# Optimization experiments

Hardware: AMD Instinct MI355X
Metric: run time of the kernel (lower is better)

## Reference

```python
import jax, jax.numpy as jnp
import numpy as np

B, NPG, DEG = 32, 1024, 16          # graphs, nodes/graph, avg degree
N, E = B * NPG, B * NPG * DEG        # 32768 nodes, 524288 edges
IN_C, HID, H, EDGE_D = 128, 64, 4, 8
RATIO = 0.5
K = int(np.ceil(RATIO * NPG))        # 512 nodes kept per graph (static)
SLOPE = 0.2                          # PyG GATConv LeakyReLU default


def setup_inputs() -> dict:
    key = jax.random.key(0)
    ks = jax.random.split(key, 10)
    x = jax.random.normal(ks[0], (N, IN_C), jnp.float32)
    # edges confined within each graph (block structure like PyG Batch)
    src_l = jax.random.randint(ks[1], (B, NPG * DEG), 0, NPG)
    dst_l = jax.random.randint(ks[2], (B, NPG * DEG), 0, NPG)
    off = (jnp.arange(B) * NPG)[:, None]
    edge_index = jnp.stack([(src_l + off).reshape(-1), (dst_l + off).reshape(-1)]).astype(jnp.int64)
    edge = jax.random.normal(ks[3], (E, EDGE_D), jnp.float32)
    batch_index = jnp.repeat(jnp.arange(B), NPG).astype(jnp.int64)
    s_in = 1.0 / np.sqrt(IN_C)
    W = jax.random.normal(ks[4], (IN_C, H, HID), jnp.float32) * s_in
    a_src = jax.random.normal(ks[5], (H, HID), jnp.float32) * s_in
    a_dst = jax.random.normal(ks[6], (H, HID), jnp.float32) * s_in
    b_gat = jnp.zeros((H * HID,), jnp.float32)
    W_lin = jax.random.normal(ks[7], (H * HID, HID), jnp.float32) * (1.0 / np.sqrt(H * HID))
    b_lin = jnp.zeros((HID,), jnp.float32)
    p_pool = jax.random.normal(ks[8], (HID,), jnp.float32)
    return dict(x=x, edge_index=edge_index, edge=edge, batch_index=batch_index,
                W=W, a_src=a_src, a_dst=a_dst, b_gat=b_gat,
                W_lin=W_lin, b_lin=b_lin, p_pool=p_pool)


def reference(x, edge_index, edge, batch_index, W, a_src, a_dst, b_gat, W_lin, b_lin, p_pool):
    n = x.shape[0]
    # --- GATConv (heads concat, self-loops added, softmax over incoming edges) ---
    loops = jnp.arange(n)
    src = jnp.concatenate([edge_index[0], loops])
    dst = jnp.concatenate([edge_index[1], loops])
    h = jnp.einsum('ni,ihc->nhc', x, W)                  # [N,H,C]
    al_src = (h * a_src).sum(-1)                          # [N,H]
    al_dst = (h * a_dst).sum(-1)                          # [N,H]
    e = jax.nn.leaky_relu(al_src[src] + al_dst[dst], SLOPE)  # [Etot,H]
    m = jax.ops.segment_max(e, dst, num_segments=n)
    ex = jnp.exp(e - m[dst])
    denom = jax.ops.segment_sum(ex, dst, num_segments=n)
    alpha = ex / denom[dst]                               # segment softmax per target
    out = jax.ops.segment_sum(h[src] * alpha[:, :, None], dst, num_segments=n)
    xg = out.reshape(n, H * HID) + b_gat
    # --- Linear ---
    xl = xg @ W_lin + b_lin                               # [N,HID]
    # --- TopKPooling (tanh(x.p/||p||) score, top ceil(ratio*n) per graph) ---
    score = jnp.tanh(xl @ p_pool / jnp.linalg.norm(p_pool))   # [N]
    topv, topi = jax.lax.top_k(score.reshape(B, NPG), K)      # [B,K]
    perm = (topi + (jnp.arange(B) * NPG)[:, None]).reshape(-1)  # global kept node ids
    xp = xl[perm] * topv.reshape(-1)[:, None]             # [B*K,HID], gated by score
    batch_out = jnp.repeat(jnp.arange(B), K)
    # edge filtering / remapping (padded with -1 instead of compacting)
    nmap = jnp.full((n,), -1, jnp.int32).at[perm].set(jnp.arange(B * K, dtype=jnp.int32))
    ns, nd = nmap[edge_index[0]], nmap[edge_index[1]]
    valid = (ns >= 0) & (nd >= 0)
    edge_index_new = jnp.where(valid, jnp.stack([ns, nd]), -1)
    edge_new = jnp.where(valid[:, None], edge, 0.0)
    # --- global mean/max pool (graphs are contiguous blocks of K nodes) ---
    xr = xp.reshape(B, K, HID)
    x1 = jnp.concatenate([xr.mean(axis=1), xr.max(axis=1)], axis=-1)  # [B,2*HID]
    return xp, edge_index_new, edge_new, batch_out, x1
```

## Files before the change

### kernel.cpp

```cpp
#include <hip/hip_runtime.h>
#include <math.h>

#define NN   32768
#define EE   524288
#define ETOT (EE + NN)
#define BB   32
#define NPG  1024
#define EPG  16384
#define RPG  17408
#define KK   512
#define INC  128
#define HID  64
#define NH   4
#define CC   256
#define SLOPE 0.2f

typedef __attribute__((ext_vector_type(8))) short short8;
typedef __attribute__((ext_vector_type(4))) float f32x4;

static __device__ inline unsigned short f2bf(float f) {
  unsigned u = __float_as_uint(f);
  unsigned r = (u + 0x7FFFu + ((u >> 16) & 1u)) >> 16;
  return (unsigned short)r;
}

__global__ __launch_bounds__(256) void prep_kernel(const float* __restrict__ W,
                                                   const float* __restrict__ a_src,
                                                   const float* __restrict__ a_dst,
                                                   const float* __restrict__ b_gat,
                                                   const float* __restrict__ W_lin,
                                                   const float* __restrict__ b_lin,
                                                   const float* __restrict__ p,
                                                   float* __restrict__ Mg,
                                                   float* __restrict__ cbuf,
                                                   unsigned short* __restrict__ Wt,
                                                   unsigned short* __restrict__ Wlt) {
  const int b = blockIdx.x, t = threadIdx.x;
  if (b >= 17) {
    int idx = (b - 17) * 256 + t;
    if (idx < 32768) {
      int c = idx >> 7, k = idx & 127;
      Wt[idx] = f2bf(W[k * 256 + c]);
    } else {
      int i2 = idx - 32768;
      int c = i2 >> 8, k = i2 & 255;
      Wlt[i2] = f2bf(W_lin[k * 64 + c]);
    }
    return;
  }
  __shared__ float pl[64];
  __shared__ float ql[256];
  __shared__ float red[256];
  __shared__ float red2[256];
  if (t < 64) pl[t] = p[t];
  __syncthreads();
  {
    float acc = 0.f;
    const float* wr = W_lin + t * 64;
#pragma unroll
    for (int c = 0; c < 64; c += 4) {
      float4 wv = *(const float4*)(wr + c);
      acc += wv.x * pl[c] + wv.y * pl[c + 1] + wv.z * pl[c + 2] + wv.w * pl[c + 3];
    }
    ql[t] = acc;
  }
  __syncthreads();
  if (b == 0) {
    float r = ql[t] * b_gat[t];
    if (t < 64) r += b_lin[t] * pl[t];
    red[t] = r;
    red2[t] = (t < 64) ? pl[t] * pl[t] : 0.f;
    __syncthreads();
    for (int s2 = 128; s2 > 0; s2 >>= 1) {
      if (t < s2) { red[t] += red[t + s2]; red2[t] += red2[t + s2]; }
      __syncthreads();
    }
    if (t == 0) { cbuf[0] = red[0]; cbuf[1] = 1.0f / sqrtf(red2[0]); }
    return;
  }
  if (t < 96) {
    const int i = (b - 1) * 8 + t / 12;
    const int j = t % 12;
    const int hh = j & 3;
    const float* wr = W + i * 256 + hh * 64;
    float acc = 0.f;
    if (j < 8) {
      const float* v = (j < 4 ? a_src : a_dst) + hh * 64;
#pragma unroll
      for (int c = 0; c < 64; c += 4) {
        float4 wv = *(const float4*)(wr + c);
        float4 vv = *(const float4*)(v + c);
        acc += wv.x * vv.x + wv.y * vv.y + wv.z * vv.z + wv.w * vv.w;
      }
    } else {
#pragma unroll
      for (int c = 0; c < 64; ++c) acc += wr[c] * ql[hh * 64 + c];
    }
    Mg[i * 12 + j] = acc;
  }
}

__global__ __launch_bounds__(256) void prep_node_kernel(const float* __restrict__ x,
                                                        const float* __restrict__ Mg,
                                                        float* __restrict__ al_s,
                                                        float* __restrict__ al_d,
                                                        float* __restrict__ hq) {
  __shared__ float xs[64][132];
  __shared__ float MsT[12][132];
  const int t = threadIdx.x;
  const int n0 = blockIdx.x * 64;
  for (int r = t; r < 1536; r += 256) MsT[r % 12][r / 12] = Mg[r];
#pragma unroll
  for (int u = 0; u < 8; ++u) {
    int idx = u * 256 + t;
    int node = idx >> 5, c4 = idx & 31;
    *(float4*)(&xs[node][c4 * 4]) =
        *(const float4*)(x + (size_t)(n0 + node) * 128 + c4 * 4);
  }
  __syncthreads();
  const int node = t >> 2, q = t & 3;
  const int j0 = q * 3;
  float a0 = 0.f, a1 = 0.f, a2 = 0.f;
#pragma unroll
  for (int c4 = 0; c4 < 32; ++c4) {
    float4 xv = *(const float4*)(&xs[node][c4 * 4]);
    float4 m0 = *(const float4*)(&MsT[j0 + 0][c4 * 4]);
    float4 m1 = *(const float4*)(&MsT[j0 + 1][c4 * 4]);
    float4 m2 = *(const float4*)(&MsT[j0 + 2][c4 * 4]);
    a0 += xv.x * m0.x + xv.y * m0.y + xv.z * m0.z + xv.w * m0.w;
    a1 += xv.x * m1.x + xv.y * m1.y + xv.z * m1.z + xv.w * m1.w;
    a2 += xv.x * m2.x + xv.y * m2.y + xv.z * m2.z + xv.w * m2.w;
  }
  const int n = n0 + node;
  float vals[3] = {a0, a1, a2};
#pragma unroll
  for (int k = 0; k < 3; ++k) {
    int j = j0 + k;
    float* base = (j < 4) ? al_s : ((j < 8) ? al_d : hq);
    int jj = (j < 4) ? j : ((j < 8) ? j - 4 : j - 8);
    base[n * 4 + jj] = vals[k];
  }
}

__global__ __launch_bounds__(256) void gemm1_kernel(const float* __restrict__ x,
                                                    const unsigned short* __restrict__ Wt,
                                                    unsigned short* __restrict__ hbf) {
  const int lane = threadIdx.x & 63;
  const int wv = threadIdx.x >> 6;
  const int q = lane >> 4, nh = lane & 15;
  const int lid = blockIdx.x;
  const int node = ((lid & 7) * 64 + (lid >> 3)) * 64 + wv * 16 + nh;
  f32x4 acc[16];
#pragma unroll
  for (int mt = 0; mt < 16; ++mt) acc[mt] = (f32x4){0.f, 0.f, 0.f, 0.f};
  const float* xr = x + (size_t)node * 128;
#pragma unroll
  for (int kc = 0; kc < 4; ++kc) {
    const float* xp = xr + kc * 32 + q * 8;
    float4 v0 = *(const float4*)(xp);
    float4 v1 = *(const float4*)(xp + 4);
    short8 b;
    b[0] = (short)f2bf(v0.x); b[1] = (short)f2bf(v0.y);
    b[2] = (short)f2bf(v0.z); b[3] = (short)f2bf(v0.w);
    b[4] = (short)f2bf(v1.x); b[5] = (short)f2bf(v1.y);
    b[6] = (short)f2bf(v1.z); b[7] = (short)f2bf(v1.w);
#pragma unroll
    for (int mt = 0; mt < 16; ++mt) {
      short8 a = *(const short8*)(Wt + (size_t)(mt * 16 + nh) * 128 + kc * 32 + q * 8);
      acc[mt] = __builtin_amdgcn_mfma_f32_16x16x32_bf16(a, b, acc[mt], 0, 0, 0);
    }
  }
  unsigned short* hr = hbf + (size_t)node * 256;
#pragma unroll
  for (int mt = 0; mt < 16; ++mt) {
    ushort4 o;
    o.x = f2bf(acc[mt][0]); o.y = f2bf(acc[mt][1]);
    o.z = f2bf(acc[mt][2]); o.w = f2bf(acc[mt][3]);
    *(ushort4*)(hr + mt * 16 + q * 4) = o;
  }
}

__global__ __launch_bounds__(1024) void scan_scatter_kernel(const int* __restrict__ ei,
                                                            int* __restrict__ row_ptr,
                                                            int* __restrict__ col) {
  __shared__ int hist[NPG];
  __shared__ int sums[NPG];
  __shared__ int lpos[NPG];
  const int b = blockIdx.x, t = threadIdx.x;
  hist[t] = 0;
  __syncthreads();
  const int e0 = b * EPG;
  for (int k = t; k < EPG; k += 1024)
    atomicAdd(&hist[ei[EE + e0 + k] - b * NPG], 1);
  __syncthreads();
  const int c = hist[t] + 1;
  sums[t] = c;
  __syncthreads();
  for (int off = 1; off < NPG; off <<= 1) {
    int v = (t >= off) ? sums[t - off] : 0;
    __syncthreads();
    sums[t] += v;
    __syncthreads();
  }
  const int excl = sums[t] - c;
  row_ptr[b * NPG + t] = b * RPG + excl;
  lpos[t] = excl;
  if (b == 0 && t == 0) row_ptr[NN] = ETOT;
  __syncthreads();
  {
    int p0 = atomicAdd(&lpos[t], 1);
    col[b * RPG + p0] = b * NPG + t;
  }
  for (int k = t; k < EPG; k += 1024) {
    int s = ei[e0 + k];
    int d = ei[EE + e0 + k];
    int p1 = atomicAdd(&lpos[d - b * NPG], 1);
    col[b * RPG + p1] = s;
  }
}

__global__ __launch_bounds__(256) void agg_kernel(const unsigned short* __restrict__ h,
                                                  const float* __restrict__ al_s,
                                                  const float* __restrict__ al_d,
                                                  const float* __restrict__ hq,
                                                  const int* __restrict__ row_ptr,
                                                  const int* __restrict__ col,
                                                  const float* __restrict__ b_gat,
                                                  const float* __restrict__ cbuf,
                                                  unsigned short* __restrict__ outg,
                                                  float* __restrict__ score) {
  __shared__ float wsh[4][256];
  __shared__ float qsh[4][256];
  __shared__ int   osh[4][64];
  const int lane = threadIdx.x & 63;
  const int wv = threadIdx.x >> 6;
  const int hqi = lane >> 4;
  const int xcd = blockIdx.x & 7;
  const int jb = blockIdx.x >> 3;
  const int n = (xcd * 1024 + jb) * 4 + wv;
  const int beg = row_ptr[n], end = row_ptr[n + 1];
  const float4 ad4 = *(const float4*)(al_d + (size_t)n * 4);
  const char* hbase = (const char*)h + (size_t)lane * 8;
  float ax = 0.f, ay = 0.f, az = 0.f, aw = 0.f, den = 0.f, sq = 0.f;
  for (int base = beg; base < end; base += 64) {
    const int rem = end - base;
    const int cnt = rem < 64 ? rem : 64;
    if (lane < cnt) {
      const int c = col[base + lane];
      osh[wv][lane] = c << 9;
      const float4 as = *(const float4*)(al_s + (size_t)c * 4);
      float e0 = as.x + ad4.x; e0 = (e0 > 0.f) ? e0 : SLOPE * e0;
      float e1 = as.y + ad4.y; e1 = (e1 > 0.f) ? e1 : SLOPE * e1;
      float e2 = as.z + ad4.z; e2 = (e2 > 0.f) ? e2 : SLOPE * e2;
      float e3 = as.w + ad4.w; e3 = (e3 > 0.f) ? e3 : SLOPE * e3;
      *(float4*)(&wsh[wv][lane * 4]) =
          make_float4(__expf(e0), __expf(e1), __expf(e2), __expf(e3));
      *(float4*)(&qsh[wv][lane * 4]) = *(const float4*)(hq + (size_t)c * 4);
    }
    const int cm1 = cnt - 1;
    uint2 v0 = *(const uint2*)(hbase + osh[wv][0]);
    uint2 v1 = *(const uint2*)(hbase + osh[wv][1 > cm1 ? cm1 : 1]);
    uint2 v2 = *(const uint2*)(hbase + osh[wv][2 > cm1 ? cm1 : 2]);
    uint2 v3 = *(const uint2*)(hbase + osh[wv][3 > cm1 ? cm1 : 3]);
    for (int i = 0; i < cnt; ++i) {
      const float w = wsh[wv][i * 4 + hqi];
      const float hqv = qsh[wv][i * 4 + hqi];
      uint2 cur = v0; v0 = v1; v1 = v2; v2 = v3;
      int ni = i + 4; ni = ni > cm1 ? cm1 : ni;
      v3 = *(const uint2*)(hbase + osh[wv][ni]);
      den += w; sq += w * hqv;
      ax += w * __uint_as_float(cur.x << 16);
      ay += w * __uint_as_float(cur.x & 0xffff0000u);
      az += w * __uint_as_float(cur.y << 16);
      aw += w * __uint_as_float(cur.y & 0xffff0000u);
    }
  }
  const float4 bg = *(const float4*)(b_gat + lane * 4);
  ushort4 ov;
  ov.x = f2bf(ax / den + bg.x); ov.y = f2bf(ay / den + bg.y);
  ov.z = f2bf(az / den + bg.z); ov.w = f2bf(aw / den + bg.w);
  *(ushort4*)(outg + (size_t)n * 256 + lane * 4) = ov;
  float sd = sq / den;
  float s0v = __shfl(sd, 0), s1v = __shfl(sd, 16);
  float s2v = __shfl(sd, 32), s3v = __shfl(sd, 48);
  if (lane == 0)
    score[n] = tanhf((s0v + s1v + s2v + s3v + cbuf[0]) * cbuf[1]);
}

__device__ inline unsigned long long shflx64(unsigned long long v, int m) {
  int lo = __shfl_xor((int)(unsigned)v, m, 64);
  int hi = __shfl_xor((int)(unsigned)(v >> 32), m, 64);
  return ((unsigned long long)(unsigned)hi << 32) | (unsigned)lo;
}

__global__ __launch_bounds__(1024) void topk_kernel(const float* __restrict__ score,
                                                    int* __restrict__ pidx_g,
                                                    float* __restrict__ tvs_g,
                                                    int* __restrict__ nmap,
                                                    float* __restrict__ out_batch) {
  __shared__ float scv[NPG];
  __shared__ unsigned long long keys[NPG];
  const int b = blockIdx.x, t = threadIdx.x;
  float sc = score[b * NPG + t];
  scv[t] = sc;
  nmap[b * NPG + t] = -1;
  unsigned long long v;
  {
    unsigned u = __float_as_uint(sc);
    u = (u & 0x80000000u) ? ~u : (u | 0x80000000u);
    u = ~u;
    v = ((unsigned long long)u << 32) | (unsigned)t;
  }
  __syncthreads();
  for (int k = 2; k <= NPG; k <<= 1) {
    for (int j = k >> 1; j > 0; j >>= 1) {
      unsigned long long pv;
      if (j >= 64) {
        keys[t] = v;
        __syncthreads();
        pv = keys[t ^ j];
        __syncthreads();
      } else {
        pv = shflx64(v, j);
      }
      bool up = ((t & k) == 0);
      bool small_side = ((t & j) == 0);
      bool take_min = (small_side == up);
      v = take_min ? (v < pv ? v : pv) : (v > pv ? v : pv);
    }
  }
  if (t < KK) {
    int idx = (int)(v & 0xFFFFFFFFull);
    pidx_g[b * KK + t] = idx;
    tvs_g[b * KK + t] = scv[idx];
    nmap[b * NPG + idx] = b * KK + t;
    out_batch[b * KK + t] = (float)b;
  }
}

__global__ __launch_bounds__(256) void gemm2xp_kernel(const unsigned short* __restrict__ outg,
                                                      const unsigned short* __restrict__ Wlt,
                                                      const float* __restrict__ bl,
                                                      const int* __restrict__ pidx_g,
                                                      const float* __restrict__ tvs_g,
                                                      float* __restrict__ out_xp) {
  const int lane = threadIdx.x & 63, wv = threadIdx.x >> 6;
  const int q = lane >> 4, nh = lane & 15;
  const int g = blockIdx.x >> 3, o = blockIdx.x & 7;
  const int r = o * 64 + wv * 16 + nh;
  const int gnode = g * NPG + pidx_g[g * KK + r];
  const float tv = tvs_g[g * KK + r];
  f32x4 acc[4];
#pragma unroll
  for (int mt = 0; mt < 4; ++mt) acc[mt] = (f32x4){0.f, 0.f, 0.f, 0.f};
  const unsigned short* ar = outg + (size_t)gnode * 256;
#pragma unroll
  for (int kc = 0; kc < 8; ++kc) {
    short8 bf = *(const short8*)(ar + kc * 32 + q * 8);
#pragma unroll
    for (int mt = 0; mt < 4; ++mt) {
      short8 a = *(const short8*)(Wlt + (size_t)(mt * 16 + nh) * 256 + kc * 32 + q * 8);
      acc[mt] = __builtin_amdgcn_mfma_f32_16x16x32_bf16(a, bf, acc[mt], 0, 0, 0);
    }
  }
#pragma unroll
  for (int mt = 0; mt < 4; ++mt) {
    const int c4 = mt * 16 + q * 4;
    float4 bl4 = *(const float4*)(bl + c4);
    float4 o4 = make_float4((acc[mt][0] + bl4.x) * tv, (acc[mt][1] + bl4.y) * tv,
                            (acc[mt][2] + bl4.z) * tv, (acc[mt][3] + bl4.w) * tv);
    *(float4*)(out_xp + (size_t)(g * KK + r) * HID + c4) = o4;
  }
}

__global__ __launch_bounds__(1024) void pool_kernel(const float* __restrict__ out_xp,
                                                    float* __restrict__ out_x1) {
  __shared__ float ps[16][64];
  __shared__ float pm[16][64];
  const int b = blockIdx.x, t = threadIdx.x;
  const int c = t & 63, rg = t >> 6;
  float s = 0.f, m = -INFINITY;
  for (int row = rg; row < KK; row += 16) {
    float vv = out_xp[(size_t)(b * KK + row) * HID + c];
    s += vv; m = fmaxf(m, vv);
  }
  ps[rg][c] = s; pm[rg][c] = m;
  __syncthreads();
  if (t < 64) {
    float st = 0.f, mt = -INFINITY;
#pragma unroll
    for (int g2 = 0; g2 < 16; ++g2) { st += ps[g2][t]; mt = fmaxf(mt, pm[g2][t]); }
    out_x1[b * 128 + t] = st * (1.0f / KK);
    out_x1[b * 128 + 64 + t] = mt;
  }
}

__global__ void edge_out_kernel(const int* __restrict__ ei, const float* __restrict__ edge,
                                const int* __restrict__ nmap,
                                float* __restrict__ out_ei, float* __restrict__ out_edge) {
  int e = blockIdx.x * 256 + threadIdx.x;
  if (e >= EE) return;
  int s = ei[e], d = ei[EE + e];
  int ns = nmap[s], nd = nmap[d];
  bool valid = (ns >= 0) && (nd >= 0);
  out_ei[e] = (float)(valid ? ns : -1);
  out_ei[EE + e] = (float)(valid ? nd : -1);
  const float4* ef = (const float4*)(edge + (size_t)e * 8);
  float4 z = make_float4(0.f, 0.f, 0.f, 0.f);
  float4 v0 = valid ? ef[0] : z;
  float4 v1 = valid ? ef[1] : z;
  float4* eo = (float4*)(out_edge + (size_t)e * 8);
  eo[0] = v0; eo[1] = v1;
}

extern "C" void kernel_launch(void* const* d_in, const int* in_sizes, int n_in,
                              void* d_out, int out_size, void* d_ws, size_t ws_size,
                              hipStream_t stream) {
  const float* x      = (const float*)d_in[0];
  const int*   ei     = (const int*)d_in[1];
  const float* edge   = (const float*)d_in[2];
  const float* W      = (const float*)d_in[4];
  const float* a_src  = (const float*)d_in[5];
  const float* a_dst  = (const float*)d_in[6];
  const float* b_gat  = (const float*)d_in[7];
  const float* W_lin  = (const float*)d_in[8];
  const float* b_lin  = (const float*)d_in[9];
  const float* p_pool = (const float*)d_in[10];

  char* ws = (char*)d_ws;
  size_t off = 0;
  auto alloc = [&](size_t bytes) -> void* {
    void* p = ws + off;
    off += (bytes + 255) & ~(size_t)255;
    return p;
  };
  unsigned short* hbf  = (unsigned short*)alloc((size_t)NN * CC * 2);
  unsigned short* outg = (unsigned short*)alloc((size_t)NN * CC * 2);
  float* al_s    = (float*)alloc((size_t)NN * NH * 4);
  float* al_d    = (float*)alloc((size_t)NN * NH * 4);
  float* hq      = (float*)alloc((size_t)NN * NH * 4);
  float* score   = (float*)alloc((size_t)NN * 4);
  int*   row_ptr = (int*)alloc((size_t)(NN + 1) * 4);
  int*   col     = (int*)alloc((size_t)ETOT * 4);
  int*   nmap    = (int*)alloc((size_t)NN * 4);
  int*   pidx_g  = (int*)alloc((size_t)BB * KK * 4);
  float* tvs_g   = (float*)alloc((size_t)BB * KK * 4);
  unsigned short* Wt  = (unsigned short*)alloc((size_t)CC * INC * 2);
  unsigned short* Wlt = (unsigned short*)alloc((size_t)HID * CC * 2);
  float* Mg      = (float*)alloc((size_t)INC * 12 * 4);
  float* cbuf    = (float*)alloc(2 * 4);

  float* out_xp    = (float*)d_out;
  float* out_ei    = out_xp + (size_t)BB * KK * HID;
  float* out_edge  = out_ei + 2 * (size_t)EE;
  float* out_batch = out_edge + (size_t)EE * 8;
  float* out_x1    = out_batch + (size_t)BB * KK;

  prep_kernel<<<209, 256, 0, stream>>>(W, a_src, a_dst, b_gat, W_lin, b_lin,
                                       p_pool, Mg, cbuf, Wt, Wlt);
  prep_node_kernel<<<NN / 64, 256, 0, stream>>>(x, Mg, al_s, al_d, hq);
  gemm1_kernel<<<512, 256, 0, stream>>>(x, Wt, hbf);
  scan_scatter_kernel<<<BB, 1024, 0, stream>>>(ei, row_ptr, col);
  agg_kernel<<<NN / 4, 256, 0, stream>>>(hbf, al_s, al_d, hq, row_ptr, col,
                                         b_gat, cbuf, outg, score);
  topk_kernel<<<BB, 1024, 0, stream>>>(score, pidx_g, tvs_g, nmap, out_batch);
  gemm2xp_kernel<<<256, 256, 0, stream>>>(outg, Wlt, b_lin, pidx_g, tvs_g, out_xp);
  pool_kernel<<<BB, 1024, 0, stream>>>(out_xp, out_x1);
  edge_out_kernel<<<(EE + 255) / 256, 256, 0, stream>>>(ei, edge, nmap, out_ei, out_edge);
}
```

Baseline: 233.1 us.

## Replace bitonic top-k sort with rank counting and use wave-shuffle scan

The per-graph top-k moves from a 1024-element bitonic sort, which needs many block-wide barriers, to a direct rank computation: each thread counts how many scores beat its own, with ties broken by index, and writes itself to that rank. The CSR scan kernel swaps a shared-memory Hillis-Steele scan with a barrier at every step for a wavefront shuffle scan plus a small cross-wave scan. Both changes cut barriers and shared-memory round trips. The rank approach does O(N^2) comparisons per graph, about 1M per block, read through LDS broadcasts.

```diff
diff --git a/kernel.cpp b/kernel.cpp
--- a/kernel.cpp
+++ b/kernel.cpp
@@ -184,9 +184,10 @@
                                                             int* __restrict__ row_ptr,
                                                             int* __restrict__ col) {
   __shared__ int hist[NPG];
-  __shared__ int sums[NPG];
   __shared__ int lpos[NPG];
+  __shared__ int wsum[16];
   const int b = blockIdx.x, t = threadIdx.x;
+  const int lane = t & 63, wid = t >> 6;
   hist[t] = 0;
   __syncthreads();
   const int e0 = b * EPG;
@@ -194,15 +195,26 @@
     atomicAdd(&hist[ei[EE + e0 + k] - b * NPG], 1);
   __syncthreads();
   const int c = hist[t] + 1;
-  sums[t] = c;
-  __syncthreads();
-  for (int off = 1; off < NPG; off <<= 1) {
-    int v = (t >= off) ? sums[t - off] : 0;
-    __syncthreads();
-    sums[t] += v;
-    __syncthreads();
-  }
-  const int excl = sums[t] - c;
+  int inc = c;
+#pragma unroll
+  for (int off = 1; off < 64; off <<= 1) {
+    int u = __shfl_up(inc, off, 64);
+    if (lane >= off) inc += u;
+  }
+  if (lane == 63) wsum[wid] = inc;
+  __syncthreads();
+  if (wid == 0) {
+    int v = (lane < 16) ? wsum[lane] : 0;
+#pragma unroll
+    for (int off = 1; off < 16; off <<= 1) {
+      int u = __shfl_up(v, off, 64);
+      if (lane >= off) v += u;
+    }
+    if (lane < 16) wsum[lane] = v;
+  }
+  __syncthreads();
+  const int woff = (wid == 0) ? 0 : wsum[wid - 1];
+  const int excl = woff + inc - c;
   row_ptr[b * NPG + t] = b * RPG + excl;
   lpos[t] = excl;
   if (b == 0 && t == 0) row_ptr[NN] = ETOT;
@@ -287,54 +299,32 @@
     score[n] = tanhf((s0v + s1v + s2v + s3v + cbuf[0]) * cbuf[1]);
 }
 
-__device__ inline unsigned long long shflx64(unsigned long long v, int m) {
-  int lo = __shfl_xor((int)(unsigned)v, m, 64);
-  int hi = __shfl_xor((int)(unsigned)(v >> 32), m, 64);
-  return ((unsigned long long)(unsigned)hi << 32) | (unsigned)lo;
-}
-
 __global__ __launch_bounds__(1024) void topk_kernel(const float* __restrict__ score,
                                                     int* __restrict__ pidx_g,
                                                     float* __restrict__ tvs_g,
                                                     int* __restrict__ nmap,
                                                     float* __restrict__ out_batch) {
   __shared__ float scv[NPG];
-  __shared__ unsigned long long keys[NPG];
   const int b = blockIdx.x, t = threadIdx.x;
-  float sc = score[b * NPG + t];
+  const float sc = score[b * NPG + t];
   scv[t] = sc;
   nmap[b * NPG + t] = -1;
-  unsigned long long v;
-  {
-    unsigned u = __float_as_uint(sc);
-    u = (u & 0x80000000u) ? ~u : (u | 0x80000000u);
-    u = ~u;
-    v = ((unsigned long long)u << 32) | (unsigned)t;
-  }
-  __syncthreads();
-  for (int k = 2; k <= NPG; k <<= 1) {
-    for (int j = k >> 1; j > 0; j >>= 1) {
-      unsigned long long pv;
-      if (j >= 64) {
-        keys[t] = v;
-        __syncthreads();
-        pv = keys[t ^ j];
-        __syncthreads();
-      } else {
-        pv = shflx64(v, j);
-      }
-      bool up = ((t & k) == 0);
-      bool small_side = ((t & j) == 0);
-      bool take_min = (small_side == up);
-      v = take_min ? (v < pv ? v : pv) : (v > pv ? v : pv);
-    }
-  }
-  if (t < KK) {
-    int idx = (int)(v & 0xFFFFFFFFull);
-    pidx_g[b * KK + t] = idx;
-    tvs_g[b * KK + t] = scv[idx];
-    nmap[b * NPG + idx] = b * KK + t;
-    out_batch[b * KK + t] = (float)b;
+  __syncthreads();
+  int rank = 0;
+#pragma unroll 4
+  for (int j4 = 0; j4 < NPG / 4; ++j4) {
+    const float4 s4 = *(const float4*)(&scv[j4 * 4]);
+    const int j = j4 * 4;
+    rank += (s4.x > sc) || (s4.x == sc && (j + 0) < t);
+    rank += (s4.y > sc) || (s4.y == sc && (j + 1) < t);
+    rank += (s4.z > sc) || (s4.z == sc && (j + 2) < t);
+    rank += (s4.w > sc) || (s4.w == sc && (j + 3) < t);
+  }
+  if (rank < KK) {
+    pidx_g[b * KK + rank] = t;
+    tvs_g[b * KK + rank] = sc;
+    nmap[b * NPG + t] = b * KK + rank;
+    out_batch[b * KK + rank] = (float)b;
   }
 }
 
```

After: 264.2 us. +13.4%, slower.
